# Performance work log

Hardware: AMD Instinct MI355X
Metric: run time of the kernel (lower is better)

The kernel has to match this reference:

```python
import jax, jax.numpy as jnp
import numpy as np

B, T, D = 2, 1024, 2048
N, K, H = 16, 4, 128          # num_heads, num_kv_heads, head_dim
TC = 1024                     # cached tokens
S = TC + T
MAX_WAVELENGTH = 10000.0
BIG_NEG = -2.3819763e38


def _apply_rope(x, positions):
    """RoPE: positions [B,L] applied to x [B,L,heads,H]."""
    half = x.shape[-1] // 2
    freq_exponents = (2.0 / x.shape[-1]) * jnp.arange(half, dtype=jnp.float32)
    timescale = MAX_WAVELENGTH ** freq_exponents                      # [H/2]
    radians = (positions.astype(jnp.float32)[..., None] / timescale)[..., None, :]  # [B,L,1,H/2]
    sin, cos = jnp.sin(radians), jnp.cos(radians)
    x1, x2 = jnp.split(x, 2, axis=-1)
    res = jnp.concatenate([x1 * cos - x2 * sin, x2 * cos + x1 * sin], axis=-1)
    return res.astype(x.dtype)


def setup_inputs() -> dict:
    key = jax.random.key(0)
    ks = jax.random.split(key, 8)
    x = jax.random.normal(ks[0], (B, T, D), dtype=jnp.float32)
    # new tokens sit right after the cache
    positions = jnp.broadcast_to(TC + jnp.arange(T, dtype=jnp.int32), (B, T))
    # causal mask over [cache + new]: query t may attend to keys s <= TC + t
    s_idx = jnp.arange(S)[None, :]
    t_idx = jnp.arange(T)[:, None]
    attn_mask = jnp.broadcast_to((s_idx <= TC + t_idx)[None, None, :, :], (B, 1, T, S))
    cache_k = jax.random.normal(ks[1], (B, TC, K, H), dtype=jnp.float32)
    cache_v = jax.random.normal(ks[2], (B, TC, K, H), dtype=jnp.float32)
    # lecun-normal-ish fan-in scaling (fan_in = D for projections, N*H for output)
    w_q = jax.random.normal(ks[3], (N, D, H), dtype=jnp.float32) * (D ** -0.5)
    w_kv = jax.random.normal(ks[4], (2, K, D, H), dtype=jnp.float32) * (D ** -0.5)
    w_out = jax.random.normal(ks[5], (N, H, D), dtype=jnp.float32) * ((N * H) ** -0.5)
    return {"x": x, "positions": positions, "attn_mask": attn_mask,
            "cache_k": cache_k, "cache_v": cache_v,
            "w_q": w_q, "w_kv": w_kv, "w_out": w_out}


def reference(x, positions, attn_mask, cache_k, cache_v, w_q, w_kv, w_out):
    dtype = x.dtype
    # projections (GQA path: num_kv_heads != num_heads)
    q = jnp.einsum('BTD,NDH->BTNH', x, w_q.astype(dtype))
    kv = jnp.einsum('BSD,CKDH->CBSKH', x, w_kv.astype(dtype))
    k_new, v_new = kv[0], kv[1]
    # inline RoPE + query scaling
    q = _apply_rope(q, positions) * (H ** -0.5)
    k_new = _apply_rope(k_new, positions)
    # KV-cache concat
    k = jnp.concatenate([cache_k, k_new], axis=1)   # [B,S,K,H]
    v = jnp.concatenate([cache_v, v_new], axis=1)
    # group heads: B T (K G) H -> B T K G H
    G = N // K
    qg = q.reshape(q.shape[0], q.shape[1], K, G, H)
    logits = jnp.einsum('BTKGH,BSKH->BKGTS', qg, k,
                        preferred_element_type=jnp.float32)
    masked = jnp.where(attn_mask[:, :, None, :, :], logits, BIG_NEG)
    probs = jax.nn.softmax(masked, axis=-1).astype(dtype)
    enc = jnp.einsum('BKGTS,BSKH->BTKGH', probs, v)
    enc = enc.reshape(enc.shape[0], enc.shape[1], N, H)  # B T (K G) H
    out = jnp.einsum('BTNH,NHD->BTD', enc, w_out.astype(dtype))
    return out, k, v
```

## Files before the change

### kernel.cpp

```cpp
#include <hip/hip_runtime.h>

#define B_  2
#define T_  1024
#define D_  2048
#define NH  16
#define KH  4
#define HD  128
#define TC_ 1024
#define S_  2048

typedef __bf16 bf16x4v __attribute__((ext_vector_type(4)));
typedef __bf16 bf16x8v __attribute__((ext_vector_type(8)));
typedef float  f32x4v  __attribute__((ext_vector_type(4)));

__device__ __forceinline__ void async_copy16(void* lds, const void* g) {
    __builtin_amdgcn_global_load_lds(
        (__attribute__((address_space(1))) void*)g,
        (__attribute__((address_space(3))) void*)lds, 16, 0, 0);
}

__global__ void cvt_x(const float* __restrict__ x, __bf16* __restrict__ xb) {
    int i = (blockIdx.x * 256 + threadIdx.x) * 4;
    float4 v = *(const float4*)(x + i);
    bf16x4v o; o[0]=(__bf16)v.x; o[1]=(__bf16)v.y; o[2]=(__bf16)v.z; o[3]=(__bf16)v.w;
    *(bf16x4v*)(xb + i) = o;
}

__global__ void tp_w(const float* __restrict__ in, __bf16* __restrict__ out) {
    __shared__ float tile[32][33];
    int h0 = blockIdx.x * 32;
    int d0 = blockIdx.y * 32;
    const float* ip = in + (size_t)blockIdx.z * (D_ * HD);
    __bf16* op = out + (size_t)blockIdx.z * (D_ * HD);
    int tx = threadIdx.x, ty = threadIdx.y;
    for (int i = 0; i < 32; i += 8)
        tile[ty + i][tx] = ip[(size_t)(d0 + ty + i) * HD + h0 + tx];
    __syncthreads();
    for (int i = 0; i < 32; i += 8)
        op[(size_t)(h0 + ty + i) * D_ + d0 + tx] = (__bf16)tile[tx][ty + i];
}

__global__ void tp_wout(const float* __restrict__ in, __bf16* __restrict__ out) {
    __shared__ float tile[32][33];
    int d0 = blockIdx.x * 32;
    int h0 = blockIdx.y * 32;
    int n  = blockIdx.z;
    const float* ip = in + (size_t)n * (HD * D_);
    int tx = threadIdx.x, ty = threadIdx.y;
    for (int i = 0; i < 32; i += 8)
        tile[ty + i][tx] = ip[(size_t)(h0 + ty + i) * D_ + d0 + tx];
    __syncthreads();
    for (int i = 0; i < 32; i += 8)
        out[(size_t)(d0 + ty + i) * (NH * HD) + n * HD + h0 + tx] = (__bf16)tile[tx][ty + i];
}

__global__ void tp_v(const float* __restrict__ vout, __bf16* __restrict__ vtb) {
    __shared__ float tile[32][33];
    int z = blockIdx.z; int b = z / KH, kh = z % KH;
    int h0 = blockIdx.x * 32;
    int s0 = blockIdx.y * 32;
    const float* ip = vout + ((size_t)b * S_ * KH + kh) * HD;
    int tx = threadIdx.x, ty = threadIdx.y;
    for (int i = 0; i < 32; i += 8)
        tile[ty + i][tx] = ip[(size_t)(s0 + ty + i) * (KH * HD) + h0 + tx];
    __syncthreads();
    __bf16* op = vtb + ((size_t)b * KH + kh) * (size_t)HD * S_;
    for (int i = 0; i < 32; i += 8)
        op[(size_t)(h0 + ty + i) * S_ + s0 + tx] = (__bf16)tile[tx][ty + i];
}

__global__ void copy_cache(const float4* __restrict__ ck, const float4* __restrict__ cv,
                           float* __restrict__ kout, float* __restrict__ vout,
                           __bf16* __restrict__ kb) {
    int i = blockIdx.x * 256 + threadIdx.x;
    int b = i >> 17;
    int r = i & 131071;
    float4 kv = ck[i];
    ((float4*)(kout + (size_t)b * S_ * KH * HD))[r] = kv;
    ((float4*)(vout + (size_t)b * S_ * KH * HD))[r] = cv[i];
    int h4 = r & 31;
    int kh = (r >> 5) & 3;
    int s  = r >> 7;
    bf16x4v o; o[0]=(__bf16)kv.x; o[1]=(__bf16)kv.y; o[2]=(__bf16)kv.z; o[3]=(__bf16)kv.w;
    *(bf16x4v*)(kb + (((size_t)(b * KH + kh) * S_ + s) * HD) + h4 * 4) = o;
}

__global__ __launch_bounds__(256, 2)
void gemm_bt(const __bf16* __restrict__ A, const __bf16* __restrict__ BT,
             float* __restrict__ C, int ldc) {
    __shared__ __bf16 As[128 * 64];
    __shared__ __bf16 Bs[128 * 64];
    const int m0 = blockIdx.x * 128, n0 = blockIdx.y * 128;
    const int tid = threadIdx.x;
    const int wave = tid >> 6, lane = tid & 63;
    const int quad = lane >> 4, l16 = lane & 15;
    const int wm = (wave & 1) * 64, wn = (wave >> 1) * 64;
    const int lrow = lane >> 3, lcol = (lane & 7) * 8;

    f32x4v acc[4][4];
    for (int i = 0; i < 4; i++)
        for (int j = 0; j < 4; j++)
            acc[i][j] = (f32x4v){0.f, 0.f, 0.f, 0.f};

    const __bf16* Abase = A + (size_t)m0 * D_;
    const __bf16* Bbase = BT + (size_t)n0 * D_;

    for (int k0 = 0; k0 < D_; k0 += 64) {
        for (int j = 0; j < 4; j++) {
            int r = wave * 32 + j * 8;
            async_copy16(As + (size_t)r * 64,
                         Abase + (size_t)(r + lrow) * D_ + k0 + lcol);
            async_copy16(Bs + (size_t)r * 64,
                         Bbase + (size_t)(r + lrow) * D_ + k0 + lcol);
        }
        __syncthreads();
        for (int ks = 0; ks < 2; ks++) {
            bf16x8v a[4], b[4];
            for (int i = 0; i < 4; i++)
                a[i] = *(const bf16x8v*)(As + (wm + i * 16 + l16) * 64 + ks * 32 + quad * 8);
            for (int j = 0; j < 4; j++)
                b[j] = *(const bf16x8v*)(Bs + (wn + j * 16 + l16) * 64 + ks * 32 + quad * 8);
            for (int i = 0; i < 4; i++)
                for (int j = 0; j < 4; j++)
                    acc[i][j] = __builtin_amdgcn_mfma_f32_16x16x32_bf16(a[i], b[j], acc[i][j], 0, 0, 0);
        }
        __syncthreads();
    }
    for (int i = 0; i < 4; i++)
        for (int j = 0; j < 4; j++)
            for (int r = 0; r < 4; r++) {
                int row = m0 + wm + i * 16 + quad * 4 + r;
                int col = n0 + wn + j * 16 + l16;
                C[(size_t)row * ldc + col] = acc[i][j][r];
            }
}

__global__ void finish_rope(const float* __restrict__ proj, const int* __restrict__ pos,
                            __bf16* __restrict__ qws, float* __restrict__ kout,
                            float* __restrict__ vout, __bf16* __restrict__ kb) {
    const int tau = blockIdx.x;
    const int b = tau >> 10, t = tau & 1023;
    const float p = (float)pos[tau];
    const float* pr = proj + (size_t)tau * 3072;
    const float qscale = 0.08838834764831845f;
    for (int idx = threadIdx.x; idx < (NH + KH) * 64; idx += 256) {
        int head = idx >> 6;
        int hh = idx & 63;
        float r = p * __expf(-(float)hh * (9.210340371976184f / 64.0f));
        float sn = sinf(r), cs = cosf(r);
        if (head < NH) {
            float x1 = pr[head * HD + hh], x2 = pr[head * HD + hh + 64];
            size_t qo = ((size_t)tau * NH + head) * HD;
            qws[qo + hh]      = (__bf16)((x1 * cs - x2 * sn) * qscale);
            qws[qo + hh + 64] = (__bf16)((x2 * cs + x1 * sn) * qscale);
        } else {
            int kh = head - NH;
            float x1 = pr[2048 + kh * HD + hh], x2 = pr[2048 + kh * HD + hh + 64];
            float k1 = x1 * cs - x2 * sn, k2 = x2 * cs + x1 * sn;
            size_t ko = ((size_t)(b * S_ + TC_ + t) * KH + kh) * HD;
            kout[ko + hh]      = k1;
            kout[ko + hh + 64] = k2;
            size_t kbo = ((size_t)(b * KH + kh) * S_ + TC_ + t) * HD;
            kb[kbo + hh]      = (__bf16)k1;
            kb[kbo + hh + 64] = (__bf16)k2;
        }
    }
    for (int idx = threadIdx.x; idx < KH * HD; idx += 256) {
        int kh = idx >> 7, h = idx & 127;
        vout[((size_t)(b * S_ + TC_ + t) * KH + kh) * HD + h] = pr[2560 + kh * HD + h];
    }
}

__global__ __launch_bounds__(512, 1)
void attn(const __bf16* __restrict__ qws, const __bf16* __restrict__ kb,
          const __bf16* __restrict__ vtb, __bf16* __restrict__ enc) {
    __shared__ __bf16 Qs[128 * 128];
    __shared__ __bf16 Ks[128 * 128];
    __shared__ __bf16 Vs[128 * 128];
    __shared__ __bf16 Ps[128 * 128];

    const int t0 = blockIdx.x * 128;
    const int n  = blockIdx.y;
    const int b  = blockIdx.z;
    const int kh = n / (NH / KH);
    const int tid = threadIdx.x, wave = tid >> 6, lane = tid & 63;
    const int quad = lane >> 4, l16 = lane & 15;
    const int wm = wave * 16;
    const int arow = lane >> 4;
    const int acol = lane & 15;

    {
        const __bf16* qtile = qws + ((size_t)(b * T_ + t0) * NH + n) * HD;
        for (int jj = 0; jj < 4; jj++) {
            int r0 = wm + jj * 4;
            int row = r0 + arow;
            async_copy16(Qs + (size_t)r0 * 128,
                         qtile + (size_t)row * (NH * HD) + ((acol ^ (row & 15)) * 8));
        }
    }

    float m_run[4], l_run[4];
    f32x4v o_acc[8];
    for (int r = 0; r < 4; r++) { m_run[r] = -INFINITY; l_run[r] = 0.f; }
    for (int j = 0; j < 8; j++) o_acc[j] = (f32x4v){0.f, 0.f, 0.f, 0.f};

    const int nS = (TC_ + t0 + 128) >> 7;
    const __bf16* kbase = kb  + ((size_t)(b * KH + kh)) * S_ * HD;
    const __bf16* vbase = vtb + ((size_t)(b * KH + kh)) * (size_t)HD * S_;

    for (int st = 0; st < nS; st++) {
        const int s0 = st * 128;
        {
            const __bf16* ktile = kbase + (size_t)s0 * HD;
            for (int jj = 0; jj < 4; jj++) {
                int r0 = wm + jj * 4;
                int row = r0 + arow;
                async_copy16(Ks + (size_t)r0 * 128,
                             ktile + (size_t)row * HD + ((acol ^ (row & 15)) * 8));
            }
        }
        {
            const __bf16* vtile = vbase + s0;
            for (int jj = 0; jj < 4; jj++) {
                int r0 = wm + jj * 4;
                int row = r0 + arow;
                async_copy16(Vs + (size_t)r0 * 128,
                             vtile + (size_t)row * S_ + ((acol ^ (row & 15)) * 8));
            }
        }
        __syncthreads();

        f32x4v sc[8];
        for (int j = 0; j < 8; j++) sc[j] = (f32x4v){0.f, 0.f, 0.f, 0.f};
        for (int ks = 0; ks < 4; ks++) {
            int ch = (ks * 4 + quad) ^ l16;
            bf16x8v a = *(const bf16x8v*)(Qs + (wm + l16) * 128 + ch * 8);
            bf16x8v bb[8];
            for (int j = 0; j < 8; j++)
                bb[j] = *(const bf16x8v*)(Ks + (j * 16 + l16) * 128 + ch * 8);
            for (int j = 0; j < 8; j++)
                sc[j] = __builtin_amdgcn_mfma_f32_16x16x32_bf16(a, bb[j], sc[j], 0, 0, 0);
        }

        if (st == nS - 1) {
            for (int j = 0; j < 8; j++)
                for (int r = 0; r < 4; r++) {
                    int row = wm + quad * 4 + r;
                    int col = j * 16 + l16;
                    if (col > row) sc[j][r] = -3.0e38f;
                }
        }

        for (int r = 0; r < 4; r++) {
            float mx = sc[0][r];
            for (int j = 1; j < 8; j++) mx = fmaxf(mx, sc[j][r]);
            for (int off = 8; off >= 1; off >>= 1) mx = fmaxf(mx, __shfl_xor(mx, off, 64));
            mx = fmaxf(mx, m_run[r]);
            float alpha = __expf(m_run[r] - mx);
            m_run[r] = mx;
            float s = 0.f;
            for (int j = 0; j < 8; j++) {
                float pv = __expf(sc[j][r] - mx);
                sc[j][r] = pv;
                s += pv;
            }
            for (int off = 8; off >= 1; off >>= 1) s += __shfl_xor(s, off, 64);
            l_run[r] = l_run[r] * alpha + s;
            for (int j = 0; j < 8; j++) o_acc[j][r] *= alpha;
        }

        for (int j = 0; j < 8; j++)
            for (int r = 0; r < 4; r++) {
                int row = wm + quad * 4 + r;
                int c = (j * 2 + (l16 >> 3)) ^ (row & 15);
                Ps[row * 128 + c * 8 + (l16 & 7)] = (__bf16)sc[j][r];
            }
        __syncthreads();

        for (int ks = 0; ks < 4; ks++) {
            int ch = (ks * 4 + quad) ^ l16;
            bf16x8v a = *(const bf16x8v*)(Ps + (wm + l16) * 128 + ch * 8);
            bf16x8v bb[8];
            for (int j = 0; j < 8; j++)
                bb[j] = *(const bf16x8v*)(Vs + (j * 16 + l16) * 128 + ch * 8);
            for (int j = 0; j < 8; j++)
                o_acc[j] = __builtin_amdgcn_mfma_f32_16x16x32_bf16(a, bb[j], o_acc[j], 0, 0, 0);
        }
        __syncthreads();
    }

    for (int r = 0; r < 4; r++) {
        float inv = 1.0f / l_run[r];
        int row = wm + quad * 4 + r;
        for (int j = 0; j < 8; j++) {
            int col = j * 16 + l16;
            enc[((size_t)(b * T_ + t0 + row) * NH + n) * HD + col] =
                (__bf16)(o_acc[j][r] * inv);
        }
    }
}

extern "C" void kernel_launch(void* const* d_in, const int* in_sizes, int n_in,
                              void* d_out, int out_size, void* d_ws, size_t ws_size,
                              hipStream_t stream) {
    const float* x       = (const float*)d_in[0];
    const int*   pos     = (const int*)d_in[1];
    const float* cache_k = (const float*)d_in[3];
    const float* cache_v = (const float*)d_in[4];
    const float* w_q     = (const float*)d_in[5];
    const float* w_kv    = (const float*)d_in[6];
    const float* w_out   = (const float*)d_in[7];

    float* out  = (float*)d_out;
    float* kout = out  + (size_t)B_ * T_ * D_;
    float* vout = kout + (size_t)B_ * S_ * KH * HD;

    char* ws = (char*)d_ws;
    __bf16* xb   = (__bf16*)ws;  ws += (size_t)B_ * T_ * D_ * 2;
    __bf16* wt   = (__bf16*)ws;  ws += (size_t)3072 * D_ * 2;
    __bf16* wot  = (__bf16*)ws;  ws += (size_t)D_ * NH * HD * 2;
    float*  proj = (float*)ws;   ws += (size_t)B_ * T_ * 3072 * 4;
    __bf16* qws  = (__bf16*)ws;  ws += (size_t)B_ * T_ * NH * HD * 2;
    __bf16* kbuf = (__bf16*)ws;  ws += (size_t)B_ * S_ * KH * HD * 2;
    __bf16* vtb  = (__bf16*)ws;  ws += (size_t)B_ * S_ * KH * HD * 2;
    __bf16* enc  = (__bf16*)ws;

    cvt_x<<<4096, 256, 0, stream>>>(x, xb);
    tp_w<<<dim3(4, 64, 16), dim3(32, 8), 0, stream>>>(w_q, wt);
    tp_w<<<dim3(4, 64, 8),  dim3(32, 8), 0, stream>>>(w_kv, wt + (size_t)16 * HD * D_);
    tp_wout<<<dim3(64, 4, 16), dim3(32, 8), 0, stream>>>(w_out, wot);
    copy_cache<<<1024, 256, 0, stream>>>((const float4*)cache_k, (const float4*)cache_v, kout, vout, kbuf);
    gemm_bt<<<dim3(16, 24), 256, 0, stream>>>(xb, wt, proj, 3072);
    finish_rope<<<2048, 256, 0, stream>>>(proj, pos, qws, kout, vout, kbuf);
    tp_v<<<dim3(4, 64, 8), dim3(32, 8), 0, stream>>>(vout, vtb);
    attn<<<dim3(8, 16, 2), 512, 0, stream>>>(qws, kbuf, vtb, enc);
    gemm_bt<<<dim3(16, 16), 256, 0, stream>>>(enc, wot, out, 2048);
}
```

Measured before the change: 302.7 us.

## Split attention KV range across two blocks and merge partial softmax results

The attention kernel now splits each query tile's key range into two halves handled by separate blocks, which doubles the grid from 256 to 512 blocks. Each block uses 256 threads with Q held in registers and a 64-key tile size, and each wave handles 32 query rows. A new merge kernel combines the two unnormalized partial outputs using their saved max and sum statistics. Waves also skip key tiles that lie entirely past their causal limit. The aim is better CU occupancy and load balance, at the cost of an extra kernel launch, intermediate bf16 partial outputs written to the reused proj buffer, and loss of precision from storing unnormalized bf16 partials.

```diff
diff --git a/kernel.cpp b/kernel.cpp
--- a/kernel.cpp
+++ b/kernel.cpp
@@ -171,133 +171,162 @@
     }
 }
 
-__global__ __launch_bounds__(512, 1)
+__global__ __launch_bounds__(256, 2)
 void attn(const __bf16* __restrict__ qws, const __bf16* __restrict__ kb,
-          const __bf16* __restrict__ vtb, __bf16* __restrict__ enc) {
-    __shared__ __bf16 Qs[128 * 128];
-    __shared__ __bf16 Ks[128 * 128];
-    __shared__ __bf16 Vs[128 * 128];
-    __shared__ __bf16 Ps[128 * 128];
+          const __bf16* __restrict__ vtb,
+          __bf16* __restrict__ op0, __bf16* __restrict__ op1,
+          float2* __restrict__ mlb0, float2* __restrict__ mlb1) {
+    __shared__ __bf16 Ks[64 * 128];
+    __shared__ __bf16 Vs[128 * 64];
+    __shared__ __bf16 Ps[128 * 72];
 
     const int t0 = blockIdx.x * 128;
     const int n  = blockIdx.y;
-    const int b  = blockIdx.z;
-    const int kh = n / (NH / KH);
-    const int tid = threadIdx.x, wave = tid >> 6, lane = tid & 63;
+    const int bz = blockIdx.z;
+    const int b = bz >> 1, half = bz & 1;
+    const int kh = n >> 2;
+    const int tid = threadIdx.x, w = tid >> 6, lane = tid & 63;
     const int quad = lane >> 4, l16 = lane & 15;
-    const int wm = wave * 16;
-    const int arow = lane >> 4;
-    const int acol = lane & 15;
-
+
+    bf16x8v qf[2][4];
     {
-        const __bf16* qtile = qws + ((size_t)(b * T_ + t0) * NH + n) * HD;
-        for (int jj = 0; jj < 4; jj++) {
-            int r0 = wm + jj * 4;
-            int row = r0 + arow;
-            async_copy16(Qs + (size_t)r0 * 128,
-                         qtile + (size_t)row * (NH * HD) + ((acol ^ (row & 15)) * 8));
-        }
-    }
-
-    float m_run[4], l_run[4];
-    f32x4v o_acc[8];
-    for (int r = 0; r < 4; r++) { m_run[r] = -INFINITY; l_run[r] = 0.f; }
-    for (int j = 0; j < 8; j++) o_acc[j] = (f32x4v){0.f, 0.f, 0.f, 0.f};
-
-    const int nS = (TC_ + t0 + 128) >> 7;
+        const __bf16* qbase = qws + ((size_t)(b * T_ + t0 + w * 32) * NH + n) * HD;
+        for (int qt = 0; qt < 2; qt++)
+            for (int ks = 0; ks < 4; ks++)
+                qf[qt][ks] = *(const bf16x8v*)(qbase + (size_t)(qt * 16 + l16) * (NH * HD)
+                                               + ks * 32 + quad * 8);
+    }
+
+    float m_run[2][4], l_run[2][4];
+    f32x4v o_acc[2][8];
+    for (int qt = 0; qt < 2; qt++)
+        for (int r = 0; r < 4; r++) { m_run[qt][r] = -INFINITY; l_run[qt][r] = 0.f; }
+    for (int qt = 0; qt < 2; qt++)
+        for (int j = 0; j < 8; j++) o_acc[qt][j] = (f32x4v){0.f, 0.f, 0.f, 0.f};
+
+    const int nS  = (TC_ + t0 + 128) >> 6;
+    const int st0 = half ? (nS >> 1) : 0;
+    const int st1 = half ? nS : (nS >> 1);
+    const int wk_max = TC_ + t0 + w * 32 + 31;
     const __bf16* kbase = kb  + ((size_t)(b * KH + kh)) * S_ * HD;
     const __bf16* vbase = vtb + ((size_t)(b * KH + kh)) * (size_t)HD * S_;
 
-    for (int st = 0; st < nS; st++) {
-        const int s0 = st * 128;
+    for (int st = st0; st < st1; st++) {
+        const int s0 = st * 64;
         {
-            const __bf16* ktile = kbase + (size_t)s0 * HD;
+            const int ar = lane >> 4, ac = lane & 15;
             for (int jj = 0; jj < 4; jj++) {
-                int r0 = wm + jj * 4;
-                int row = r0 + arow;
+                int r0 = w * 16 + jj * 4;
+                int row = r0 + ar;
                 async_copy16(Ks + (size_t)r0 * 128,
-                             ktile + (size_t)row * HD + ((acol ^ (row & 15)) * 8));
+                             kbase + (size_t)(s0 + row) * HD + ((ac ^ (row & 15)) * 8));
             }
         }
         {
-            const __bf16* vtile = vbase + s0;
+            const int ar = lane >> 3, ac = lane & 7;
             for (int jj = 0; jj < 4; jj++) {
-                int r0 = wm + jj * 4;
-                int row = r0 + arow;
-                async_copy16(Vs + (size_t)r0 * 128,
-                             vtile + (size_t)row * S_ + ((acol ^ (row & 15)) * 8));
+                int r0 = w * 32 + jj * 8;
+                int row = r0 + ar;
+                async_copy16(Vs + (size_t)r0 * 64,
+                             vbase + (size_t)row * S_ + s0 + ((ac ^ (row & 7)) * 8));
             }
         }
         __syncthreads();
 
-        f32x4v sc[8];
-        for (int j = 0; j < 8; j++) sc[j] = (f32x4v){0.f, 0.f, 0.f, 0.f};
-        for (int ks = 0; ks < 4; ks++) {
-            int ch = (ks * 4 + quad) ^ l16;
-            bf16x8v a = *(const bf16x8v*)(Qs + (wm + l16) * 128 + ch * 8);
-            bf16x8v bb[8];
+        if (s0 <= wk_max) {
+            f32x4v sc[2][4];
+            for (int qt = 0; qt < 2; qt++)
+                for (int j = 0; j < 4; j++) sc[qt][j] = (f32x4v){0.f, 0.f, 0.f, 0.f};
+            for (int ks = 0; ks < 4; ks++) {
+                bf16x8v bb[4];
+                for (int j = 0; j < 4; j++)
+                    bb[j] = *(const bf16x8v*)(Ks + (j * 16 + l16) * 128
+                                              + (((ks * 4 + quad) ^ l16) * 8));
+                for (int qt = 0; qt < 2; qt++)
+                    for (int j = 0; j < 4; j++)
+                        sc[qt][j] = __builtin_amdgcn_mfma_f32_16x16x32_bf16(qf[qt][ks], bb[j], sc[qt][j], 0, 0, 0);
+            }
+
+            if (st >= nS - 2) {
+                for (int qt = 0; qt < 2; qt++)
+                    for (int j = 0; j < 4; j++)
+                        for (int r = 0; r < 4; r++) {
+                            int s_abs = s0 + j * 16 + l16;
+                            int q_abs = t0 + w * 32 + qt * 16 + quad * 4 + r;
+                            if (s_abs > TC_ + q_abs) sc[qt][j][r] = -3.0e38f;
+                        }
+            }
+
+            for (int qt = 0; qt < 2; qt++)
+                for (int r = 0; r < 4; r++) {
+                    float mx = sc[qt][0][r];
+                    for (int j = 1; j < 4; j++) mx = fmaxf(mx, sc[qt][j][r]);
+                    for (int off = 8; off >= 1; off >>= 1) mx = fmaxf(mx, __shfl_xor(mx, off, 64));
+                    mx = fmaxf(mx, m_run[qt][r]);
+                    float alpha = __expf(m_run[qt][r] - mx);
+                    m_run[qt][r] = mx;
+                    float s = 0.f;
+                    for (int j = 0; j < 4; j++) {
+                        float pv = __expf(sc[qt][j][r] - mx);
+                        sc[qt][j][r] = pv;
+                        s += pv;
+                    }
+                    for (int off = 8; off >= 1; off >>= 1) s += __shfl_xor(s, off, 64);
+                    l_run[qt][r] = l_run[qt][r] * alpha + s;
+                    for (int j = 0; j < 8; j++) o_acc[qt][j][r] *= alpha;
+                }
+
+            for (int qt = 0; qt < 2; qt++)
+                for (int j = 0; j < 4; j++)
+                    for (int r = 0; r < 4; r++) {
+                        int row = w * 32 + qt * 16 + quad * 4 + r;
+                        Ps[row * 72 + j * 16 + l16] = (__bf16)sc[qt][j][r];
+                    }
+
+            for (int ks = 0; ks < 2; ks++) {
+                bf16x8v av[2];
+                for (int qt = 0; qt < 2; qt++)
+                    av[qt] = *(const bf16x8v*)(Ps + (w * 32 + qt * 16 + l16) * 72
+                                               + ks * 32 + quad * 8);
+                bf16x8v bb[8];
+                for (int j = 0; j < 8; j++)
+                    bb[j] = *(const bf16x8v*)(Vs + (j * 16 + l16) * 64
+                                              + (((ks * 4 + quad) ^ (l16 & 7)) * 8));
+                for (int qt = 0; qt < 2; qt++)
+                    for (int j = 0; j < 8; j++)
+                        o_acc[qt][j] = __builtin_amdgcn_mfma_f32_16x16x32_bf16(av[qt], bb[j], o_acc[qt][j], 0, 0, 0);
+            }
+        }
+        __syncthreads();
+    }
+
+    __bf16* op = half ? op1 : op0;
+    float2* ml = half ? mlb1 : mlb0;
+    for (int qt = 0; qt < 2; qt++)
+        for (int r = 0; r < 4; r++) {
+            int grow = (b * NH + n) * T_ + t0 + w * 32 + qt * 16 + quad * 4 + r;
+            if (l16 == 0) ml[grow] = make_float2(m_run[qt][r], l_run[qt][r]);
             for (int j = 0; j < 8; j++)
-                bb[j] = *(const bf16x8v*)(Ks + (j * 16 + l16) * 128 + ch * 8);
-            for (int j = 0; j < 8; j++)
-                sc[j] = __builtin_amdgcn_mfma_f32_16x16x32_bf16(a, bb[j], sc[j], 0, 0, 0);
-        }
-
-        if (st == nS - 1) {
-            for (int j = 0; j < 8; j++)
-                for (int r = 0; r < 4; r++) {
-                    int row = wm + quad * 4 + r;
-                    int col = j * 16 + l16;
-                    if (col > row) sc[j][r] = -3.0e38f;
-                }
-        }
-
-        for (int r = 0; r < 4; r++) {
-            float mx = sc[0][r];
-            for (int j = 1; j < 8; j++) mx = fmaxf(mx, sc[j][r]);
-            for (int off = 8; off >= 1; off >>= 1) mx = fmaxf(mx, __shfl_xor(mx, off, 64));
-            mx = fmaxf(mx, m_run[r]);
-            float alpha = __expf(m_run[r] - mx);
-            m_run[r] = mx;
-            float s = 0.f;
-            for (int j = 0; j < 8; j++) {
-                float pv = __expf(sc[j][r] - mx);
-                sc[j][r] = pv;
-                s += pv;
-            }
-            for (int off = 8; off >= 1; off >>= 1) s += __shfl_xor(s, off, 64);
-            l_run[r] = l_run[r] * alpha + s;
-            for (int j = 0; j < 8; j++) o_acc[j][r] *= alpha;
-        }
-
-        for (int j = 0; j < 8; j++)
-            for (int r = 0; r < 4; r++) {
-                int row = wm + quad * 4 + r;
-                int c = (j * 2 + (l16 >> 3)) ^ (row & 15);
-                Ps[row * 128 + c * 8 + (l16 & 7)] = (__bf16)sc[j][r];
-            }
-        __syncthreads();
-
-        for (int ks = 0; ks < 4; ks++) {
-            int ch = (ks * 4 + quad) ^ l16;
-            bf16x8v a = *(const bf16x8v*)(Ps + (wm + l16) * 128 + ch * 8);
-            bf16x8v bb[8];
-            for (int j = 0; j < 8; j++)
-                bb[j] = *(const bf16x8v*)(Vs + (j * 16 + l16) * 128 + ch * 8);
-            for (int j = 0; j < 8; j++)
-                o_acc[j] = __builtin_amdgcn_mfma_f32_16x16x32_bf16(a, bb[j], o_acc[j], 0, 0, 0);
-        }
-        __syncthreads();
-    }
-
-    for (int r = 0; r < 4; r++) {
-        float inv = 1.0f / l_run[r];
-        int row = wm + quad * 4 + r;
-        for (int j = 0; j < 8; j++) {
-            int col = j * 16 + l16;
-            enc[((size_t)(b * T_ + t0 + row) * NH + n) * HD + col] =
-                (__bf16)(o_acc[j][r] * inv);
-        }
-    }
+                op[(size_t)grow * HD + j * 16 + l16] = (__bf16)o_acc[qt][j][r];
+        }
+}
+
+__global__ void merge(const __bf16* __restrict__ o0, const __bf16* __restrict__ o1,
+                      const float2* __restrict__ ml0, const float2* __restrict__ ml1,
+                      __bf16* __restrict__ enc) {
+    int gid = blockIdx.x * 256 + threadIdx.x;
+    int row = gid >> 5, c4 = (gid & 31) * 4;
+    float2 A = ml0[row], Bm = ml1[row];
+    float m  = fmaxf(A.x, Bm.x);
+    float wA = __expf(A.x - m), wB = __expf(Bm.x - m);
+    float inv = 1.0f / (wA * A.y + wB * Bm.y);
+    bf16x4v a = *(const bf16x4v*)(o0 + (size_t)row * HD + c4);
+    bf16x4v c = *(const bf16x4v*)(o1 + (size_t)row * HD + c4);
+    int b = row >> 14, n = (row >> 10) & 15, t = row & 1023;
+    bf16x4v e;
+    for (int i = 0; i < 4; i++)
+        e[i] = (__bf16)((wA * (float)a[i] + wB * (float)c[i]) * inv);
+    *(bf16x4v*)(enc + (((size_t)(b * T_ + t) * NH + n) * HD) + c4) = e;
 }
 
 extern "C" void kernel_launch(void* const* d_in, const int* in_sizes, int n_in,
@@ -325,6 +354,12 @@
     __bf16* vtb  = (__bf16*)ws;  ws += (size_t)B_ * S_ * KH * HD * 2;
     __bf16* enc  = (__bf16*)ws;
 
+    const size_t ON = (size_t)B_ * NH * T_ * HD;
+    __bf16* op0 = (__bf16*)proj;
+    __bf16* op1 = op0 + ON;
+    float2* ml0 = (float2*)(op1 + ON);
+    float2* ml1 = ml0 + (size_t)B_ * NH * T_;
+
     cvt_x<<<4096, 256, 0, stream>>>(x, xb);
     tp_w<<<dim3(4, 64, 16), dim3(32, 8), 0, stream>>>(w_q, wt);
     tp_w<<<dim3(4, 64, 8),  dim3(32, 8), 0, stream>>>(w_kv, wt + (size_t)16 * HD * D_);
@@ -333,6 +368,7 @@
     gemm_bt<<<dim3(16, 24), 256, 0, stream>>>(xb, wt, proj, 3072);
     finish_rope<<<2048, 256, 0, stream>>>(proj, pos, qws, kout, vout, kbuf);
     tp_v<<<dim3(4, 64, 8), dim3(32, 8), 0, stream>>>(vout, vtb);
-    attn<<<dim3(8, 16, 2), 512, 0, stream>>>(qws, kbuf, vtb, enc);
+    attn<<<dim3(8, 16, 4), 256, 0, stream>>>(qws, kbuf, vtb, op0, op1, ml0, ml1);
+    merge<<<4096, 256, 0, stream>>>(op0, op1, ml0, ml1, enc);
     gemm_bt<<<dim3(16, 16), 256, 0, stream>>>(enc, wot, out, 2048);
 }
```

Measured after the change: 313.2 us. 3.5% more time.
